# Optimization experiments

Hardware: AMD Instinct MI355X
Metric: run time of the kernel (lower is better)

## Reference

```python
import jax, jax.numpy as jnp
import numpy as np

THRESHOLD = 0.5
TEMPERATURE = 4.0
LOG_CLAMP = -100.0  # torch BCELoss clamps log terms at -100

B, C, K = 131072, 128, 64


def setup_inputs() -> dict:
    key = jax.random.key(0)
    k1, k2, k3, k4, k5 = jax.random.split(key, 5)
    # sigmoid-like probabilities in (0, 1)
    output = jax.random.uniform(k1, (B, C), dtype=jnp.float32)
    output_consistency = jax.random.uniform(k2, (B, C), dtype=jnp.float32)
    label = jax.random.uniform(k3, (B, C), dtype=jnp.float32)
    class_idx = jnp.sort(jax.random.randint(k4, (K,), 0, C)).astype(jnp.int64)
    batch_mask = jax.random.randint(k5, (B,), 0, 2).astype(bool)
    return {
        "output": output,
        "output_consistency": output_consistency,
        "label": label,
        "class_idx": class_idx,
        "batch_mask": batch_mask,
    }


def _clamped_log(x):
    return jnp.maximum(jnp.log(x), LOG_CLAMP)


def reference(output, output_consistency, label, class_idx, batch_mask):
    # gather the class columns of interest: [B, K]
    o = output[:, class_idx]
    oc = output_consistency[:, class_idx]
    y = label[:, class_idx]

    # sharpened pseudo-label (branch on threshold, fused via where)
    sharp = jnp.where(o > THRESHOLD,
                      o + (1.0 - o) / TEMPERATURE,
                      o - o / TEMPERATURE)

    # per-element BCE (torch BCELoss semantics with log clamp)
    bce = -(y * _clamped_log(o) + (1.0 - y) * _clamped_log(1.0 - o))
    pseudo = (o - sharp) ** 2          # F.mse_loss on scalars
    consistency = (oc - sharp) ** 2

    per_elem = bce + pseudo + consistency            # [B, K]
    row_mask = batch_mask.astype(per_elem.dtype)     # [B]
    total = jnp.sum(per_elem * row_mask[:, None])
    cnt = jnp.sum(row_mask) * per_elem.shape[1]
    return total / cnt
```

## Files before the change

kernel.cpp:

```cpp
#include <hip/hip_runtime.h>

#define BLOCK 256
#define GRID  1024
#define B_ROWS 131072
#define C_COLS 128
#define K_SEL  64

__global__ void init_acc(double* acc) {
    acc[0] = 0.0;
    acc[1] = 0.0;
}

__global__ __launch_bounds__(BLOCK) void semi_loss_main(
    const float* __restrict__ out,
    const float* __restrict__ outc,
    const float* __restrict__ lab,
    const int*  __restrict__ class_idx,
    const int*  __restrict__ batch_mask,
    double* __restrict__ acc)
{
    __shared__ float w[C_COLS];
    if (threadIdx.x < C_COLS) w[threadIdx.x] = 0.0f;
    __syncthreads();
    if (threadIdx.x < K_SEL) {
        int c = class_idx[threadIdx.x];
        atomicAdd(&w[c], 1.0f);
    }
    __syncthreads();

    const int total_vec = B_ROWS * C_COLS / 4;
    float sum  = 0.0f;
    float cntf = 0.0f;

    int tid    = blockIdx.x * BLOCK + threadIdx.x;
    int stride = GRID * BLOCK;

    for (int v = tid; v < total_vec; v += stride) {
        int base = v << 2;
        int row  = base >> 7;
        int col  = base & (C_COLS - 1);
        int m    = batch_mask[row];
        if (col == 0) cntf += m ? 1.0f : 0.0f;
        if (!m) continue;

        float4 o4  = ((const float4*)out )[v];
        float4 oc4 = ((const float4*)outc)[v];
        float4 y4  = ((const float4*)lab )[v];

        float ov[4]  = {o4.x,  o4.y,  o4.z,  o4.w};
        float ocv[4] = {oc4.x, oc4.y, oc4.z, oc4.w};
        float yv[4]  = {y4.x,  y4.y,  y4.z,  y4.w};

        #pragma unroll
        for (int j = 0; j < 4; ++j) {
            float wc = w[col + j];
            float o  = ov[j];
            float oc = ocv[j];
            float y  = yv[j];

            float sharp = (o > 0.5f) ? (o + (1.0f - o) * 0.25f)
                                     : (o - o * 0.25f);
            float lo  = fmaxf(logf(o),        -100.0f);
            float l1o = fmaxf(logf(1.0f - o), -100.0f);
            float bce = -(y * lo + (1.0f - y) * l1o);

            float dp = o  - sharp;
            float dc = oc - sharp;
            float per_elem = bce + dp * dp + dc * dc;
            sum += wc * per_elem;
        }
    }

    #pragma unroll
    for (int off = 32; off > 0; off >>= 1) {
        sum  += __shfl_down(sum,  off);
        cntf += __shfl_down(cntf, off);
    }
    __shared__ float ssum[BLOCK / 64];
    __shared__ float scnt[BLOCK / 64];
    int wave = threadIdx.x >> 6;
    int lane = threadIdx.x & 63;
    if (lane == 0) { ssum[wave] = sum; scnt[wave] = cntf; }
    __syncthreads();
    if (threadIdx.x == 0) {
        float s = 0.0f, c = 0.0f;
        #pragma unroll
        for (int i = 0; i < BLOCK / 64; ++i) { s += ssum[i]; c += scnt[i]; }
        atomicAdd(&acc[0], (double)s);
        atomicAdd(&acc[1], (double)c);
    }
}

__global__ void finalize_kernel(const double* acc, float* out) {
    double cnt = acc[1] * (double)K_SEL;
    out[0] = (float)(acc[0] / cnt);
}

extern "C" void kernel_launch(void* const* d_in, const int* in_sizes, int n_in,
                              void* d_out, int out_size, void* d_ws, size_t ws_size,
                              hipStream_t stream) {
    const float* out_p  = (const float*)d_in[0];
    const float* outc_p = (const float*)d_in[1];
    const float* lab_p  = (const float*)d_in[2];
    const int*   cidx_p = (const int*)d_in[3];
    const int*   mask_p = (const int*)d_in[4];
    double* acc = (double*)d_ws;

    init_acc<<<1, 1, 0, stream>>>(acc);
    semi_loss_main<<<GRID, BLOCK, 0, stream>>>(out_p, outc_p, lab_p, cidx_p, mask_p, acc);
    finalize_kernel<<<1, 1, 0, stream>>>(acc, (float*)d_out);
}
```

Before: 201.4 us.

## Use one thread per float4 and replace atomics with two-pass partial reduction

Replaces the grid-stride loop over a fixed 1024-block grid with one thread per float4 vector, launching enough blocks to cover the whole input. Each block writes a float2 partial instead of doing double atomicAdds, and a single-block kernel reduces the partials in double precision and computes the final mean, which removes the init and finalize launches. This aims to increase memory-level parallelism and cut launch and atomic overhead. In exchange it needs a larger workspace and repeats the shared weight-table setup in every one of many more blocks.

```diff
diff --git a/kernel.cpp b/kernel.cpp
--- a/kernel.cpp
+++ b/kernel.cpp
@@ -1,15 +1,12 @@
 #include <hip/hip_runtime.h>
 
-#define BLOCK 256
-#define GRID  1024
+#define BLOCK  256
 #define B_ROWS 131072
 #define C_COLS 128
 #define K_SEL  64
+#define TOTAL_VEC (B_ROWS * C_COLS / 4)
+#define GRID (TOTAL_VEC / BLOCK)
 
-__global__ void init_acc(double* acc) {
-    acc[0] = 0.0;
-    acc[1] = 0.0;
-}
 
 __global__ __launch_bounds__(BLOCK) void semi_loss_main(
     const float* __restrict__ out,
@@ -17,7 +14,7 @@
     const float* __restrict__ lab,
     const int*  __restrict__ class_idx,
     const int*  __restrict__ batch_mask,
-    double* __restrict__ acc)
+    float2* __restrict__ partials)
 {
     __shared__ float w[C_COLS];
     if (threadIdx.x < C_COLS) w[threadIdx.x] = 0.0f;
@@ -28,21 +25,17 @@
     }
     __syncthreads();
 
-    const int total_vec = B_ROWS * C_COLS / 4;
+    const int v   = blockIdx.x * BLOCK + threadIdx.x;
+    const int row = v >> 5;
+    const int c4  = v & 31;
+    const int col = c4 << 2;
+
+    const int m = batch_mask[row];
+
     float sum  = 0.0f;
-    float cntf = 0.0f;
+    float cntf = (c4 == 0 && m) ? 1.0f : 0.0f;
 
-    int tid    = blockIdx.x * BLOCK + threadIdx.x;
-    int stride = GRID * BLOCK;
-
-    for (int v = tid; v < total_vec; v += stride) {
-        int base = v << 2;
-        int row  = base >> 7;
-        int col  = base & (C_COLS - 1);
-        int m    = batch_mask[row];
-        if (col == 0) cntf += m ? 1.0f : 0.0f;
-        if (!m) continue;
-
+    if (m) {
         float4 o4  = ((const float4*)out )[v];
         float4 oc4 = ((const float4*)outc)[v];
         float4 y4  = ((const float4*)lab )[v];
@@ -66,8 +59,7 @@
 
             float dp = o  - sharp;
             float dc = oc - sharp;
-            float per_elem = bce + dp * dp + dc * dc;
-            sum += wc * per_elem;
+            sum += wc * (bce + dp * dp + dc * dc);
         }
     }
 
@@ -86,14 +78,36 @@
         float s = 0.0f, c = 0.0f;
         #pragma unroll
         for (int i = 0; i < BLOCK / 64; ++i) { s += ssum[i]; c += scnt[i]; }
-        atomicAdd(&acc[0], (double)s);
-        atomicAdd(&acc[1], (double)c);
+        partials[blockIdx.x] = make_float2(s, c);
     }
 }
 
-__global__ void finalize_kernel(const double* acc, float* out) {
-    double cnt = acc[1] * (double)K_SEL;
-    out[0] = (float)(acc[0] / cnt);
+__global__ __launch_bounds__(BLOCK) void semi_loss_reduce(
+    const float2* __restrict__ partials, float* __restrict__ out)
+{
+    double s = 0.0, c = 0.0;
+    for (int i = threadIdx.x; i < GRID; i += BLOCK) {
+        float2 p = partials[i];
+        s += (double)p.x;
+        c += (double)p.y;
+    }
+    #pragma unroll
+    for (int off = 32; off > 0; off >>= 1) {
+        s += __shfl_down(s, off);
+        c += __shfl_down(c, off);
+    }
+    __shared__ double dsum[BLOCK / 64];
+    __shared__ double dcnt[BLOCK / 64];
+    int wave = threadIdx.x >> 6;
+    int lane = threadIdx.x & 63;
+    if (lane == 0) { dsum[wave] = s; dcnt[wave] = c; }
+    __syncthreads();
+    if (threadIdx.x == 0) {
+        double ts = 0.0, tc = 0.0;
+        #pragma unroll
+        for (int i = 0; i < BLOCK / 64; ++i) { ts += dsum[i]; tc += dcnt[i]; }
+        out[0] = (float)(ts / (tc * (double)K_SEL));
+    }
 }
 
 extern "C" void kernel_launch(void* const* d_in, const int* in_sizes, int n_in,
@@ -104,9 +118,9 @@
     const float* lab_p  = (const float*)d_in[2];
     const int*   cidx_p = (const int*)d_in[3];
     const int*   mask_p = (const int*)d_in[4];
-    double* acc = (double*)d_ws;
+    float2* partials = (float2*)d_ws;
 
-    init_acc<<<1, 1, 0, stream>>>(acc);
-    semi_loss_main<<<GRID, BLOCK, 0, stream>>>(out_p, outc_p, lab_p, cidx_p, mask_p, acc);
-    finalize_kernel<<<1, 1, 0, stream>>>(acc, (float*)d_out);
+    semi_loss_main<<<GRID, BLOCK, 0, stream>>>(out_p, outc_p, lab_p,
+                                               cidx_p, mask_p, partials);
+    semi_loss_reduce<<<1, BLOCK, 0, stream>>>(partials, (float*)d_out);
 }
```

After: 194.4 us. 1.04x faster.
